# Optimization experiments

Measured on AMD Instinct MI355X. Metric: run time of the kernel, lower is better.

Reference implementation:

```python
import jax, jax.numpy as jnp
import numpy as np

N, S, C, K, V = 8, 2048, 4, 512, 64


def setup_inputs() -> dict:
    key = jax.random.key(0)
    kx, ke = jax.random.split(key)
    x = jax.random.normal(kx, (N, S, C, V), dtype=jnp.float32)
    # nn.Parameter(torch.rand(...)) -> uniform [0,1)
    embedding = jax.random.uniform(ke, (C, K, V), dtype=jnp.float32)
    return {"x": x, "embedding": embedding}


def reference(x, embedding):
    n, s, c, v = x.shape
    xf = x.reshape(n * s, c, v)  # (NS, C, V)
    x2 = jnp.sum(xf * xf, axis=-1, keepdims=True)           # (NS, C, 1)
    e2 = jnp.sum(embedding * embedding, axis=-1)            # (C, K)
    xe = jnp.einsum('ncv,ckv->nck', xf, embedding)          # (NS, C, K)
    d2 = x2 - 2.0 * xe + e2[None]                           # (NS, C, K)
    index = jnp.argmin(d2, axis=2)                          # (NS, C)
    # gather: output[n, c] = embedding[c, index[n, c]]
    output = embedding[jnp.arange(c)[None, :], index]       # (NS, C, V)
    output = output.reshape(x.shape)
    out0 = jax.lax.stop_gradient(output - x) + x            # straight-through
    d1 = jax.lax.stop_gradient(x) - output
    out1 = jnp.sum(d1 * d1, axis=3)                         # (N, S, C)
    d2_ = x - jax.lax.stop_gradient(output)
    out2 = jnp.sum(d2_ * d2_, axis=3)                       # (N, S, C)
    return (out0, out1, out2)
```

## Files before the change

kernel.cpp:

```cpp
#include <hip/hip_runtime.h>

#define NROW 16384
#define CCH  4
#define KCB  512
#define VDIM 64

typedef __attribute__((ext_vector_type(8))) short  short8;
typedef __attribute__((ext_vector_type(4))) float  floatx4;

__device__ inline unsigned short bf16h(float v, float* rem) {
    unsigned u = __float_as_uint(v);
    unsigned r = u + 0x7FFFu + ((u >> 16) & 1u);
    unsigned short h = (unsigned short)(r >> 16);
    *rem = v - __uint_as_float((unsigned)h << 16);
    return h;
}

__global__ __launch_bounds__(256, 2)
void vq_fused(const float* __restrict__ x, const float* __restrict__ emb,
              float* __restrict__ out) {
    __shared__ unsigned short btile[2][2048];
    __shared__ float e2s[KCB];

    const int tid  = threadIdx.x;
    const int lane = tid & 63;
    const int m    = lane & 15;
    const int quad = lane >> 4;
    const int wave = tid >> 6;
    const int c    = blockIdx.y;
    const int rbase = blockIdx.x * 128 + wave * 32;

    const float* embc = emb + (size_t)c * (KCB * VDIM);

    for (int cc = tid; cc < KCB; cc += 256) {
        const float4* ep = (const float4*)(embc + (size_t)cc * VDIM);
        float s = 0.f;
#pragma unroll
        for (int i = 0; i < 16; ++i) {
            const float4 t = ep[i];
            s = fmaf(t.x, t.x, s); s = fmaf(t.y, t.y, s);
            s = fmaf(t.z, t.z, s); s = fmaf(t.w, t.w, s);
        }
        e2s[cc] = s;
    }

    short8 ah[2][2], al[2][2];
#pragma unroll
    for (int g = 0; g < 2; ++g) {
        const int row = rbase + g * 16 + m;
        const float4* xr = (const float4*)(x + ((size_t)row * CCH + c) * VDIM);
#pragma unroll
        for (int h = 0; h < 2; ++h) {
            const float4 f0 = xr[h * 8 + quad * 2];
            const float4 f1 = xr[h * 8 + quad * 2 + 1];
            const float fv[8] = {f0.x, f0.y, f0.z, f0.w, f1.x, f1.y, f1.z, f1.w};
            short8 hh, ll;
#pragma unroll
            for (int j = 0; j < 8; ++j) {
                float r, d;
                hh[j] = (short)bf16h(fv[j], &r);
                ll[j] = (short)bf16h(r, &d);
            }
            ah[g][h] = hh; al[g][h] = ll;
        }
    }

    {
        const float4 t0 = ((const float4*)embc)[tid];
        const int code = tid >> 4, f4 = tid & 15;
        ushort4 h4, l4; float r, d;
        h4.x = bf16h(t0.x, &r); l4.x = bf16h(r, &d);
        h4.y = bf16h(t0.y, &r); l4.y = bf16h(r, &d);
        h4.z = bf16h(t0.z, &r); l4.z = bf16h(r, &d);
        h4.w = bf16h(t0.w, &r); l4.w = bf16h(r, &d);
        const int off = (f4 >> 1) * 128 + code * 8 + (f4 & 1) * 4;
        *(ushort4*)&btile[0][off]        = h4;
        *(ushort4*)&btile[0][1024 + off] = l4;
    }
    __syncthreads();

    float bd[2][4]; int bkk[2][4];
#pragma unroll
    for (int g = 0; g < 2; ++g)
#pragma unroll
        for (int j = 0; j < 4; ++j) { bd[g][j] = 3.4e38f; bkk[g][j] = 0; }

    for (int t = 0; t < KCB / 16; ++t) {
        const int cur = t & 1;
        float4 nt;
        if (t < 31) nt = ((const float4*)(embc + (size_t)(t + 1) * 16 * VDIM))[tid];

        const unsigned short* bt = btile[cur];
        const short8 bh0 = *(const short8*)&bt[      quad * 128 + m * 8];
        const short8 bh1 = *(const short8*)&bt[(4 + quad) * 128 + m * 8];
        const short8 bl0 = *(const short8*)&bt[1024 +       quad * 128 + m * 8];
        const short8 bl1 = *(const short8*)&bt[1024 + (4 + quad) * 128 + m * 8];
        const float e2v = e2s[t * 16 + m];

        floatx4 acc0 = {0.f, 0.f, 0.f, 0.f}, acc1 = {0.f, 0.f, 0.f, 0.f};
        acc0 = __builtin_amdgcn_mfma_f32_16x16x32_bf16(ah[0][0], bh0, acc0, 0, 0, 0);
        acc1 = __builtin_amdgcn_mfma_f32_16x16x32_bf16(ah[1][0], bh0, acc1, 0, 0, 0);
        acc0 = __builtin_amdgcn_mfma_f32_16x16x32_bf16(ah[0][1], bh1, acc0, 0, 0, 0);
        acc1 = __builtin_amdgcn_mfma_f32_16x16x32_bf16(ah[1][1], bh1, acc1, 0, 0, 0);
        acc0 = __builtin_amdgcn_mfma_f32_16x16x32_bf16(ah[0][0], bl0, acc0, 0, 0, 0);
        acc1 = __builtin_amdgcn_mfma_f32_16x16x32_bf16(ah[1][0], bl0, acc1, 0, 0, 0);
        acc0 = __builtin_amdgcn_mfma_f32_16x16x32_bf16(ah[0][1], bl1, acc0, 0, 0, 0);
        acc1 = __builtin_amdgcn_mfma_f32_16x16x32_bf16(ah[1][1], bl1, acc1, 0, 0, 0);
        acc0 = __builtin_amdgcn_mfma_f32_16x16x32_bf16(al[0][0], bh0, acc0, 0, 0, 0);
        acc1 = __builtin_amdgcn_mfma_f32_16x16x32_bf16(al[1][0], bh0, acc1, 0, 0, 0);
        acc0 = __builtin_amdgcn_mfma_f32_16x16x32_bf16(al[0][1], bh1, acc0, 0, 0, 0);
        acc1 = __builtin_amdgcn_mfma_f32_16x16x32_bf16(al[1][1], bh1, acc1, 0, 0, 0);

        const int code = t * 16 + m;
#pragma unroll
        for (int j = 0; j < 4; ++j) {
            const float d0 = fmaf(-2.0f, acc0[j], e2v);
            const float d1 = fmaf(-2.0f, acc1[j], e2v);
            if (d0 < bd[0][j]) { bd[0][j] = d0; bkk[0][j] = code; }
            if (d1 < bd[1][j]) { bd[1][j] = d1; bkk[1][j] = code; }
        }

        if (t < 31) {
            const int codew = tid >> 4, f4 = tid & 15;
            ushort4 h4, l4; float r, d;
            h4.x = bf16h(nt.x, &r); l4.x = bf16h(r, &d);
            h4.y = bf16h(nt.y, &r); l4.y = bf16h(r, &d);
            h4.z = bf16h(nt.z, &r); l4.z = bf16h(r, &d);
            h4.w = bf16h(nt.w, &r); l4.w = bf16h(r, &d);
            const int off = (f4 >> 1) * 128 + codew * 8 + (f4 & 1) * 4;
            *(ushort4*)&btile[cur ^ 1][off]        = h4;
            *(ushort4*)&btile[cur ^ 1][1024 + off] = l4;
        }
        __syncthreads();
    }

#pragma unroll
    for (int g = 0; g < 2; ++g)
#pragma unroll
    for (int j = 0; j < 4; ++j) {
        float d = bd[g][j]; int k = bkk[g][j];
#pragma unroll
        for (int mask = 1; mask < 16; mask <<= 1) {
            const float od = __shfl_xor(d, mask, 64);
            const int   ok = __shfl_xor(k, mask, 64);
            if (od < d || (od == d && ok < k)) { d = od; k = ok; }
        }
        bd[g][j] = d; bkk[g][j] = k;
    }

    const size_t base1 = (size_t)NROW * CCH * VDIM;
    const size_t base2 = base1 + (size_t)NROW * CCH;
#pragma unroll
    for (int g = 0; g < 2; ++g)
#pragma unroll
    for (int j = 0; j < 4; ++j) {
        const int row  = rbase + g * 16 + quad * 4 + j;
        const int code = bkk[g][j];
        const float4 t4 = ((const float4*)(x + ((size_t)row * CCH + c) * VDIM))[m];
        const float4 e4 = ((const float4*)(embc + (size_t)code * VDIM))[m];
        float4 w;
        w.x = (e4.x - t4.x) + t4.x;
        w.y = (e4.y - t4.y) + t4.y;
        w.z = (e4.z - t4.z) + t4.z;
        w.w = (e4.w - t4.w) + t4.w;
        ((float4*)(out + ((size_t)row * CCH + c) * VDIM))[m] = w;
        float s = 0.f, dx;
        dx = t4.x - e4.x; s = fmaf(dx, dx, s);
        dx = t4.y - e4.y; s = fmaf(dx, dx, s);
        dx = t4.z - e4.z; s = fmaf(dx, dx, s);
        dx = t4.w - e4.w; s = fmaf(dx, dx, s);
        s += __shfl_xor(s, 1, 64);
        s += __shfl_xor(s, 2, 64);
        s += __shfl_xor(s, 4, 64);
        s += __shfl_xor(s, 8, 64);
        if (m == 0) {
            const size_t idx = (size_t)row * CCH + c;
            out[base1 + idx] = s;
            out[base2 + idx] = s;
        }
    }
}

extern "C" void kernel_launch(void* const* d_in, const int* in_sizes, int n_in,
                              void* d_out, int out_size, void* d_ws, size_t ws_size,
                              hipStream_t stream) {
    const float* x   = (const float*)d_in[0];
    const float* emb = (const float*)d_in[1];
    float* out = (float*)d_out;
    vq_fused<<<dim3(NROW / 128, CCH), dim3(256), 0, stream>>>(x, emb, out);
}
```

Baseline: 100.00 us.

## Stage whole per-channel codebook in LDS once and drop per-tile barriers

Each block now converts the whole 512-code codebook for its channel into bf16 hi/lo halves in shared memory up front, computing code norms with a wave shuffle reduction. The 32-step loop then runs without any global loads or __syncthreads. Blocks grow to 512 threads covering 256 rows with one block per CU, and the MFMA chain is split into two independent accumulators to shorten dependency chains. The cost is about 130 KB of LDS per block, which limits occupancy to one block per CU and adds a large startup phase before compute begins.

Measured after the change: 92.62 us. 7.4% less time.

```diff
diff --git a/kernel.cpp b/kernel.cpp
--- a/kernel.cpp
+++ b/kernel.cpp
@@ -4,6 +4,7 @@
 #define CCH  4
 #define KCB  512
 #define VDIM 64
+#define KO   4096
 
 typedef __attribute__((ext_vector_type(8))) short  short8;
 typedef __attribute__((ext_vector_type(4))) float  floatx4;
@@ -16,11 +17,13 @@
     return h;
 }
 
-__global__ __launch_bounds__(256, 2)
+__global__ __launch_bounds__(512, 1)
 void vq_fused(const float* __restrict__ x, const float* __restrict__ emb,
               float* __restrict__ out) {
-    __shared__ unsigned short btile[2][2048];
-    __shared__ float e2s[KCB];
+    extern __shared__ unsigned short smem[];
+    unsigned short* bhi = smem;
+    unsigned short* blo = smem + 32768;
+    float* e2s = (float*)(smem + 65536);
 
     const int tid  = threadIdx.x;
     const int lane = tid & 63;
@@ -28,20 +31,35 @@
     const int quad = lane >> 4;
     const int wave = tid >> 6;
     const int c    = blockIdx.y;
-    const int rbase = blockIdx.x * 128 + wave * 32;
+    const int rbase = blockIdx.x * 256 + wave * 32;
 
     const float* embc = emb + (size_t)c * (KCB * VDIM);
 
-    for (int cc = tid; cc < KCB; cc += 256) {
-        const float4* ep = (const float4*)(embc + (size_t)cc * VDIM);
-        float s = 0.f;
+    {
+        const int cb = wave * 64;
 #pragma unroll
-        for (int i = 0; i < 16; ++i) {
-            const float4 t = ep[i];
+        for (int j = 0; j < 16; ++j) {
+            const int g = cb * 16 + j * 64 + lane;
+            const float4 t = ((const float4*)embc)[g];
+            const int code = cb + j * 4 + quad;
+            const int koct = m >> 1, half = m & 1;
+            ushort4 h4, l4; float r, d;
+            h4.x = bf16h(t.x, &r); l4.x = bf16h(r, &d);
+            h4.y = bf16h(t.y, &r); l4.y = bf16h(r, &d);
+            h4.z = bf16h(t.z, &r); l4.z = bf16h(r, &d);
+            h4.w = bf16h(t.w, &r); l4.w = bf16h(r, &d);
+            const int off = (koct * 512 + code) * 8 + half * 4;
+            *(ushort4*)&bhi[off] = h4;
+            *(ushort4*)&blo[off] = l4;
+            float s = 0.f;
             s = fmaf(t.x, t.x, s); s = fmaf(t.y, t.y, s);
             s = fmaf(t.z, t.z, s); s = fmaf(t.w, t.w, s);
+            s += __shfl_xor(s, 1, 64);
+            s += __shfl_xor(s, 2, 64);
+            s += __shfl_xor(s, 4, 64);
+            s += __shfl_xor(s, 8, 64);
+            if (m == 0) e2s[code] = s;
         }
-        e2s[cc] = s;
     }
 
     short8 ah[2][2], al[2][2];
@@ -65,18 +83,6 @@
         }
     }
 
-    {
-        const float4 t0 = ((const float4*)embc)[tid];
-        const int code = tid >> 4, f4 = tid & 15;
-        ushort4 h4, l4; float r, d;
-        h4.x = bf16h(t0.x, &r); l4.x = bf16h(r, &d);
-        h4.y = bf16h(t0.y, &r); l4.y = bf16h(r, &d);
-        h4.z = bf16h(t0.z, &r); l4.z = bf16h(r, &d);
-        h4.w = bf16h(t0.w, &r); l4.w = bf16h(r, &d);
-        const int off = (f4 >> 1) * 128 + code * 8 + (f4 & 1) * 4;
-        *(ushort4*)&btile[0][off]        = h4;
-        *(ushort4*)&btile[0][1024 + off] = l4;
-    }
     __syncthreads();
 
     float bd[2][4]; int bkk[2][4];
@@ -85,53 +91,39 @@
 #pragma unroll
         for (int j = 0; j < 4; ++j) { bd[g][j] = 3.4e38f; bkk[g][j] = 0; }
 
+#pragma unroll 4
     for (int t = 0; t < KCB / 16; ++t) {
-        const int cur = t & 1;
-        float4 nt;
-        if (t < 31) nt = ((const float4*)(embc + (size_t)(t + 1) * 16 * VDIM))[tid];
+        const int code = t * 16 + m;
+        const unsigned short* ph = bhi + (size_t)(quad * 512 + code) * 8;
+        const unsigned short* pl = blo + (size_t)(quad * 512 + code) * 8;
+        const short8 bh0 = *(const short8*)ph;
+        const short8 bh1 = *(const short8*)(ph + 4 * KO);
+        const short8 bl0 = *(const short8*)pl;
+        const short8 bl1 = *(const short8*)(pl + 4 * KO);
+        const float e2v = e2s[code];
 
-        const unsigned short* bt = btile[cur];
-        const short8 bh0 = *(const short8*)&bt[      quad * 128 + m * 8];
-        const short8 bh1 = *(const short8*)&bt[(4 + quad) * 128 + m * 8];
-        const short8 bl0 = *(const short8*)&bt[1024 +       quad * 128 + m * 8];
-        const short8 bl1 = *(const short8*)&bt[1024 + (4 + quad) * 128 + m * 8];
-        const float e2v = e2s[t * 16 + m];
+        floatx4 acch0 = {0.f,0.f,0.f,0.f}, acch1 = {0.f,0.f,0.f,0.f};
+        floatx4 accm0 = {0.f,0.f,0.f,0.f}, accm1 = {0.f,0.f,0.f,0.f};
+        acch0 = __builtin_amdgcn_mfma_f32_16x16x32_bf16(ah[0][0], bh0, acch0, 0, 0, 0);
+        acch1 = __builtin_amdgcn_mfma_f32_16x16x32_bf16(ah[1][0], bh0, acch1, 0, 0, 0);
+        accm0 = __builtin_amdgcn_mfma_f32_16x16x32_bf16(ah[0][0], bl0, accm0, 0, 0, 0);
+        accm1 = __builtin_amdgcn_mfma_f32_16x16x32_bf16(ah[1][0], bl0, accm1, 0, 0, 0);
+        acch0 = __builtin_amdgcn_mfma_f32_16x16x32_bf16(ah[0][1], bh1, acch0, 0, 0, 0);
+        acch1 = __builtin_amdgcn_mfma_f32_16x16x32_bf16(ah[1][1], bh1, acch1, 0, 0, 0);
+        accm0 = __builtin_amdgcn_mfma_f32_16x16x32_bf16(al[0][0], bh0, accm0, 0, 0, 0);
+        accm1 = __builtin_amdgcn_mfma_f32_16x16x32_bf16(al[1][0], bh0, accm1, 0, 0, 0);
+        accm0 = __builtin_amdgcn_mfma_f32_16x16x32_bf16(ah[0][1], bl1, accm0, 0, 0, 0);
+        accm1 = __builtin_amdgcn_mfma_f32_16x16x32_bf16(ah[1][1], bl1, accm1, 0, 0, 0);
+        accm0 = __builtin_amdgcn_mfma_f32_16x16x32_bf16(al[0][1], bh1, accm0, 0, 0, 0);
+        accm1 = __builtin_amdgcn_mfma_f32_16x16x32_bf16(al[1][1], bh1, accm1, 0, 0, 0);
 
-        floatx4 acc0 = {0.f, 0.f, 0.f, 0.f}, acc1 = {0.f, 0.f, 0.f, 0.f};
-        acc0 = __builtin_amdgcn_mfma_f32_16x16x32_bf16(ah[0][0], bh0, acc0, 0, 0, 0);
-        acc1 = __builtin_amdgcn_mfma_f32_16x16x32_bf16(ah[1][0], bh0, acc1, 0, 0, 0);
-        acc0 = __builtin_amdgcn_mfma_f32_16x16x32_bf16(ah[0][1], bh1, acc0, 0, 0, 0);
-        acc1 = __builtin_amdgcn_mfma_f32_16x16x32_bf16(ah[1][1], bh1, acc1, 0, 0, 0);
-        acc0 = __builtin_amdgcn_mfma_f32_16x16x32_bf16(ah[0][0], bl0, acc0, 0, 0, 0);
-        acc1 = __builtin_amdgcn_mfma_f32_16x16x32_bf16(ah[1][0], bl0, acc1, 0, 0, 0);
-        acc0 = __builtin_amdgcn_mfma_f32_16x16x32_bf16(ah[0][1], bl1, acc0, 0, 0, 0);
-        acc1 = __builtin_amdgcn_mfma_f32_16x16x32_bf16(ah[1][1], bl1, acc1, 0, 0, 0);
-        acc0 = __builtin_amdgcn_mfma_f32_16x16x32_bf16(al[0][0], bh0, acc0, 0, 0, 0);
-        acc1 = __builtin_amdgcn_mfma_f32_16x16x32_bf16(al[1][0], bh0, acc1, 0, 0, 0);
-        acc0 = __builtin_amdgcn_mfma_f32_16x16x32_bf16(al[0][1], bh1, acc0, 0, 0, 0);
-        acc1 = __builtin_amdgcn_mfma_f32_16x16x32_bf16(al[1][1], bh1, acc1, 0, 0, 0);
-
-        const int code = t * 16 + m;
 #pragma unroll
         for (int j = 0; j < 4; ++j) {
-            const float d0 = fmaf(-2.0f, acc0[j], e2v);
-            const float d1 = fmaf(-2.0f, acc1[j], e2v);
+            const float d0 = fmaf(-2.0f, acch0[j] + accm0[j], e2v);
+            const float d1 = fmaf(-2.0f, acch1[j] + accm1[j], e2v);
             if (d0 < bd[0][j]) { bd[0][j] = d0; bkk[0][j] = code; }
             if (d1 < bd[1][j]) { bd[1][j] = d1; bkk[1][j] = code; }
         }
-
-        if (t < 31) {
-            const int codew = tid >> 4, f4 = tid & 15;
-            ushort4 h4, l4; float r, d;
-            h4.x = bf16h(nt.x, &r); l4.x = bf16h(r, &d);
-            h4.y = bf16h(nt.y, &r); l4.y = bf16h(r, &d);
-            h4.z = bf16h(nt.z, &r); l4.z = bf16h(r, &d);
-            h4.w = bf16h(nt.w, &r); l4.w = bf16h(r, &d);
-            const int off = (f4 >> 1) * 128 + codew * 8 + (f4 & 1) * 4;
-            *(ushort4*)&btile[cur ^ 1][off]        = h4;
-            *(ushort4*)&btile[cur ^ 1][1024 + off] = l4;
-        }
-        __syncthreads();
     }
 
 #pragma unroll
@@ -187,5 +179,6 @@
     const float* x   = (const float*)d_in[0];
     const float* emb = (const float*)d_in[1];
     float* out = (float*)d_out;
-    vq_fused<<<dim3(NROW / 128, CCH), dim3(256), 0, stream>>>(x, emb, out);
+    const size_t lds_bytes = 65536u * 2u + 512u * 4u;
+    vq_fused<<<dim3(NROW / 256, CCH), dim3(512), lds_bytes, stream>>>(x, emb, out);
 }
```
